# Optimization experiments

Measured on AMD Instinct MI355X. Metric: run time of the kernel, lower is better.

## Reference

```python
import jax, jax.numpy as jnp
import numpy as np

N = 16000      # points
K = 16         # neighbors per query (fixed-degree CSR)
M = N * K      # attention pairs
C = 384        # embed_dim
H = 6          # num_heads
HD = C // H    # head_dim = 64
L = 25         # quant_grid_length = window/quant = 6.0/0.24
T2 = 2 * L - 1 # rel-pos table length = 49
WIN = 6.0
QUANT = 0.24
SCALE = HD ** -0.5


def setup_inputs() -> dict:
    key = jax.random.key(0)
    ks = jax.random.split(key, 12)
    feats = jax.random.normal(ks[0], (N, C), jnp.float32)
    xyz = jax.random.uniform(ks[1], (N, 3), jnp.float32) * 240.0
    index_0 = jnp.repeat(jnp.arange(N, dtype=jnp.int32), K)            # sorted query ids per pair
    index_0_offsets = jnp.arange(0, M + 1, K, dtype=jnp.int32)         # CSR offsets
    index_1 = jax.random.randint(ks[2], (M,), 0, N, jnp.int32)         # key ids per pair
    sort_idx = jax.random.permutation(ks[3], N).astype(jnp.int32)
    lin = lambda k: jax.random.normal(k, (C, C), jnp.float32) * 0.02
    tab = lambda k: jax.random.normal(k, (T2, 3, H, HD), jnp.float32) * 0.02
    return {
        'feats': feats, 'xyz': xyz,
        'index_0': index_0, 'index_0_offsets': index_0_offsets,
        'index_1': index_1, 'sort_idx': sort_idx,
        'Wq': lin(ks[4]), 'bq': jnp.zeros((C,), jnp.float32),
        'Wk': lin(ks[5]), 'bk': jnp.zeros((C,), jnp.float32),
        'Wv': lin(ks[6]), 'bv': jnp.zeros((C,), jnp.float32),
        'Wp': lin(ks[7]), 'bp': jnp.zeros((C,), jnp.float32),
        'Tq': tab(ks[8]), 'Tk': tab(ks[9]), 'Tv': tab(ks[10]),
    }


def reference(feats, xyz, index_0, index_0_offsets, index_1, sort_idx,
              Wq, bq, Wk, bk, Wv, bv, Wp, bp, Tq, Tk, Tv):
    n = feats.shape[0]
    # QKV projections (key/value default to query feats in the module)
    q = (feats @ Wq.T + bq).reshape(n, H, HD) * SCALE
    k = (feats @ Wk.T + bk).reshape(n, H, HD)
    v = (feats @ Wv.T + bv).reshape(n, H, HD)
    # sort into contiguous-window order
    qs, ks_, vs = q[sort_idx], k[sort_idx], v[sort_idx]
    xyz_s = xyz[sort_idx]
    # quantized in-window coords (shift_win=False -> shift 0)
    xq = jnp.floor(((xyz_s - xyz_s.min(0)) % WIN) / QUANT)             # [N,3], values in [0, L-1]
    i0, i1 = index_0, index_1
    rel_idx = (xq[i0] - xq[i1]).astype(jnp.int32) + (L - 1)            # [M,3] in [0, 2L-2]
    # attention logits: q.k plus contextual relative-position terms
    attn = jnp.einsum('mhd,mhd->mh', qs[i0], ks_[i1])                  # [M,H]
    for t in range(3):
        dq = jnp.einsum('nhd,lhd->nlh', qs, Tq[:, t])                  # [N,T2,H]
        dk = jnp.einsum('nhd,lhd->nlh', ks_, Tk[:, t])
        attn = attn + dq[i0, rel_idx[:, t]] + dk[i1, rel_idx[:, t]]
    # scatter softmax over CSR segments (segments given by index_0)
    amax = jax.ops.segment_max(attn, i0, num_segments=n)
    e = jnp.exp(attn - amax[i0])
    denom = jax.ops.segment_sum(e, i0, num_segments=n)
    a = e / denom[i0]                                                  # [M,H]
    # weighted value aggregation
    x = jax.ops.segment_sum(a[:, :, None] * vs[i1], i0, num_segments=n)  # [N,H,HD]
    # relative-position value contribution, factored through table bins
    for t in range(3):
        seg2 = i0 * T2 + rel_idx[:, t]
        w = jax.ops.segment_sum(a, seg2, num_segments=n * T2).reshape(n, T2, H)
        x = x + jnp.einsum('nlh,lhd->nhd', w, Tv[:, t])
    # unsort back to input order and project
    out = jnp.zeros_like(x).at[sort_idx].set(x).reshape(n, C)
    return out @ Wp.T + bp
```

## Files before the change

### kernel.cpp

```cpp
#include <hip/hip_runtime.h>
#include <hip/hip_bf16.h>
#include <cstdint>
#include <cstddef>

#define NPTS 16000
#define KNB  16
#define CDIM 384
#define NH   6
#define HDIM 64
#define T2C  49
#define NL3T 147
#define THR  160
#define NXC  1152
#define KVROW 384

static constexpr float WIN    = 6.0f;
static constexpr float QUANT  = 0.24f;
static constexpr float QSCALE = 0.125f;
static constexpr float DQS    = 8.0f;
static constexpr float DQSINV = 0.125f;

typedef __attribute__((ext_vector_type(8))) short short8;
typedef __attribute__((ext_vector_type(4))) float floatx4;
typedef __attribute__((ext_vector_type(4))) unsigned short ushort4v;
typedef __attribute__((ext_vector_type(2))) float float2v;

__device__ inline unsigned short f2bf(float x) {
    unsigned int u = __float_as_uint(x);
    unsigned int r = (u + 0x7fffu + ((u >> 16) & 1u)) >> 16;
    return (unsigned short)r;
}
__device__ inline float bf2f(unsigned short b) {
    return __uint_as_float(((unsigned int)b) << 16);
}
__device__ inline float f8tof(unsigned char b) {
    return __builtin_amdgcn_cvt_f32_fp8((int)b, 0);
}
__device__ inline float2v bfpair(unsigned int w) {
    float2v r;
    r.x = __uint_as_float(w << 16);
    r.y = __uint_as_float(w & 0xffff0000u);
    return r;
}

__device__ inline void swz_nh(int& nb, int& h) {
    const int gx   = gridDim.x;
    const int nwg  = gx * NH;
    const int orig = blockIdx.y * gx + blockIdx.x;
    const int q    = nwg >> 3, r = nwg & 7;
    const int xcd  = orig & 7, idx = orig >> 3;
    const int wg   = (xcd < r ? xcd * (q + 1) : r * (q + 1) + (xcd - r) * q) + idx;
    h  = wg / gx;
    nb = wg % gx;
}

__global__ void min_kernel(const float* __restrict__ xyz,
                           unsigned int* __restrict__ minbits) {
    float m0 = INFINITY, m1 = INFINITY, m2 = INFINITY;
    for (int i = blockIdx.x * blockDim.x + threadIdx.x; i < NPTS;
         i += gridDim.x * blockDim.x) {
        m0 = fminf(m0, xyz[i * 3 + 0]);
        m1 = fminf(m1, xyz[i * 3 + 1]);
        m2 = fminf(m2, xyz[i * 3 + 2]);
    }
#pragma unroll
    for (int off = 1; off < 64; off <<= 1) {
        m0 = fminf(m0, __shfl_xor(m0, off, 64));
        m1 = fminf(m1, __shfl_xor(m1, off, 64));
        m2 = fminf(m2, __shfl_xor(m2, off, 64));
    }
    if ((threadIdx.x & 63) == 0) {
        atomicMin(&minbits[0], __float_as_uint(m0));
        atomicMin(&minbits[1], __float_as_uint(m1));
        atomicMin(&minbits[2], __float_as_uint(m2));
    }
}

__global__ void xq_kernel(const float* __restrict__ xyz,
                          const int* __restrict__ sort_idx,
                          const unsigned int* __restrict__ minbits,
                          int* __restrict__ xq) {
    int n = blockIdx.x * blockDim.x + threadIdx.x;
    if (n >= NPTS) return;
    int orig = sort_idx[n];
#pragma unroll
    for (int t = 0; t < 3; ++t) {
        float mn = __uint_as_float(minbits[t]);
        float v  = xyz[orig * 3 + t] - mn;
        float md = fmodf(v, WIN);
        float q  = floorf(md / QUANT);
        xq[n * 3 + t] = (int)q;
    }
}

__global__ void relpack_kernel(const int* __restrict__ idx1,
                               const int* __restrict__ xq,
                               unsigned int* __restrict__ pairs) {
    int m = blockIdx.x * blockDim.x + threadIdx.x;
    if (m >= NPTS * KNB) return;
    int n = m >> 4;
    int key = idx1[m];
    int r0 = xq[n * 3 + 0] - xq[key * 3 + 0] + 24; r0 = min(max(r0, 0), T2C - 1);
    int r1 = xq[n * 3 + 1] - xq[key * 3 + 1] + 24; r1 = min(max(r1, 0), T2C - 1);
    int r2 = xq[n * 3 + 2] - xq[key * 3 + 2] + 24; r2 = min(max(r2, 0), T2C - 1);
    pairs[m] = (unsigned)key | ((unsigned)r0 << 14) | ((unsigned)r1 << 20) |
               ((unsigned)r2 << 26);
}

#define G0 (NPTS * CDIM / 4)
#define G1 (3 * CDIM * CDIM)
#define G2 (CDIM * CDIM)
#define G3 (NH * THR * HDIM)
#define G6 (NH * THR * HDIM)
#define G7 (NH * THR * HDIM)
#define G4 (3 * CDIM)
#define G5 (CDIM)
__global__ void prep_kernel(const float* __restrict__ feats,
                            const int* __restrict__ sortix,
                            const float* __restrict__ Wq,
                            const float* __restrict__ Wk,
                            const float* __restrict__ Wv,
                            const float* __restrict__ Wp,
                            const float* __restrict__ bq,
                            const float* __restrict__ bk,
                            const float* __restrict__ bv,
                            const float* __restrict__ bp,
                            const float* __restrict__ Tv,
                            const float* __restrict__ Tq,
                            const float* __restrict__ Tk,
                            unsigned short* __restrict__ featsbf,
                            unsigned short* __restrict__ Wall,
                            unsigned short* __restrict__ Wpbf,
                            float* __restrict__ Tvh,
                            unsigned short* __restrict__ Tqh,
                            unsigned short* __restrict__ Tkh,
                            float* __restrict__ bfull,
                            float* __restrict__ bproj) {
    int i = blockIdx.x * blockDim.x + threadIdx.x;
    if (i < G0) {
        int n  = i / (CDIM / 4);
        int c4 = (i % (CDIM / 4)) * 4;
        const float4 v = *(const float4*)&feats[(size_t)sortix[n] * CDIM + c4];
        ushort4v o;
        o.x = f2bf(v.x); o.y = f2bf(v.y); o.z = f2bf(v.z); o.w = f2bf(v.w);
        *(ushort4v*)&featsbf[(size_t)n * CDIM + c4] = o;
        return;
    }
    i -= G0;
    if (i < G1) {
        int j = i / CDIM, k = i % CDIM;
        float v = (j < 384) ? Wq[j * CDIM + k]
                : (j < 768) ? Wk[(j - 384) * CDIM + k]
                            : Wv[(j - 768) * CDIM + k];
        Wall[i] = f2bf(v);
        return;
    }
    i -= G1;
    if (i < G2) { Wpbf[i] = f2bf(Wp[i]); return; }
    i -= G2;
    if (i < G3) {
        int jr = (i / HDIM) % THR, d = i % HDIM, h = i / (THR * HDIM);
        Tvh[i] = (jr < NL3T) ? Tv[(size_t)(jr * 6 + h) * HDIM + d] : 0.0f;
        return;
    }
    i -= G3;
    if (i < G6) {
        int jr = (i / HDIM) % THR, d = i % HDIM, h = i / (THR * HDIM);
        Tqh[i] = (jr < NL3T) ? f2bf(Tq[(size_t)(jr * 6 + h) * HDIM + d])
                             : (unsigned short)0;
        return;
    }
    i -= G6;
    if (i < G7) {
        int jr = (i / HDIM) % THR, d = i % HDIM, h = i / (THR * HDIM);
        Tkh[i] = (jr < NL3T) ? f2bf(Tk[(size_t)(jr * 6 + h) * HDIM + d])
                             : (unsigned short)0;
        return;
    }
    i -= G7;
    if (i < G4) {
        bfull[i] = (i < 384) ? bq[i] : (i < 768) ? bk[i - 384] : bv[i - 768];
        return;
    }
    i -= G4;
    if (i < G5) { bproj[i] = bp[i]; }
}

__global__ __launch_bounds__(256) void gemm_big(
    const unsigned short* __restrict__ Abf,
    const unsigned short* __restrict__ Wmat,
    const float* __restrict__ bias,
    int mode,
    unsigned char* __restrict__ qh8, unsigned char* __restrict__ kvh8,
    float* __restrict__ outf) {
    __shared__ unsigned short As[128 * 64];
    __shared__ unsigned short Bs[128 * 64];
    const int tid  = threadIdx.x;
    const int lane = tid & 63;
    const int w    = tid >> 6;
    const int wm   = w >> 1, wn = w & 1;

    const int nwg  = gridDim.x * gridDim.y;
    const int orig = blockIdx.y * gridDim.x + blockIdx.x;
    const int qq   = nwg >> 3, rr = nwg & 7;
    const int xcd  = orig & 7, idx = orig >> 3;
    const int wg   = (xcd < rr ? xcd * (qq + 1) : rr * (qq + 1) + (xcd - rr) * qq) + idx;
    const int jn0  = (wg % gridDim.x) * 128;
    const int m0   = (wg / gridDim.x) * 128;

    floatx4 acc[4][4];
#pragma unroll
    for (int i = 0; i < 4; ++i)
#pragma unroll
        for (int j = 0; j < 4; ++j) acc[i][j] = (floatx4)0.0f;

    for (int kt = 0; kt < 6; ++kt) {
        const int k0 = kt * 64;
#pragma unroll
        for (int q = 0; q < 4; ++q) {
            const int s    = w * 4 + q;
            const int row  = s * 8 + (lane >> 3);
            const int col  = (lane & 7) * 8;
            const unsigned short* ga = Abf  + (size_t)(m0  + row) * CDIM + k0 + col;
            const unsigned short* gb = Wmat + (size_t)(jn0 + row) * CDIM + k0 + col;
            __builtin_amdgcn_global_load_lds(
                (const __attribute__((address_space(1))) void*)ga,
                (__attribute__((address_space(3))) void*)&As[s * 512], 16, 0, 0);
            __builtin_amdgcn_global_load_lds(
                (const __attribute__((address_space(1))) void*)gb,
                (__attribute__((address_space(3))) void*)&Bs[s * 512], 16, 0, 0);
        }
        __syncthreads();
#pragma unroll
        for (int ks = 0; ks < 2; ++ks) {
            short8 a[4], b[4];
#pragma unroll
            for (int mi = 0; mi < 4; ++mi) {
                int row = wm * 64 + mi * 16 + (lane & 15);
                a[mi] = *(const short8*)&As[row * 64 + ks * 32 + (lane >> 4) * 8];
            }
#pragma unroll
            for (int ni = 0; ni < 4; ++ni) {
                int jr = wn * 64 + ni * 16 + (lane & 15);
                b[ni] = *(const short8*)&Bs[jr * 64 + ks * 32 + (lane >> 4) * 8];
            }
#pragma unroll
            for (int mi = 0; mi < 4; ++mi)
#pragma unroll
                for (int ni = 0; ni < 4; ++ni)
                    acc[mi][ni] = __builtin_amdgcn_mfma_f32_16x16x32_bf16(
                        b[ni], a[mi], acc[mi][ni], 0, 0, 0);
        }
        __syncthreads();
    }

#pragma unroll
    for (int mi = 0; mi < 4; ++mi) {
        const int n = m0 + wm * 64 + mi * 16 + (lane & 15);
#pragma unroll
        for (int ni = 0; ni < 4; ++ni) {
            const int jjb = jn0 + wn * 64 + ni * 16 + (lane >> 4) * 4;
            const float4 b4 = *(const float4*)&bias[jjb];
            const float v0 = acc[mi][ni][0] + b4.x;
            const float v1 = acc[mi][ni][1] + b4.y;
            const float v2 = acc[mi][ni][2] + b4.z;
            const float v3 = acc[mi][ni][3] + b4.w;
            if (mode == 0) {
                if (jjb < 384) {
                    const int h = jjb >> 6, d = jjb & 63;
                    ushort4v o;
                    o.x = f2bf(v0 * QSCALE); o.y = f2bf(v1 * QSCALE);
                    o.z = f2bf(v2 * QSCALE); o.w = f2bf(v3 * QSCALE);
                    *(ushort4v*)(qh8 + ((size_t)h * NPTS + n) * 128 + d * 2) = o;
                } else if (jjb < 768) {
                    const int jj = jjb - 384;
                    const int h = jj >> 6, d = jj & 63;
                    ushort4v o;
                    o.x = f2bf(v0); o.y = f2bf(v1);
                    o.z = f2bf(v2); o.w = f2bf(v3);
                    *(ushort4v*)(kvh8 + ((size_t)h * NPTS + n) * KVROW + d * 2) = o;
                } else {
                    const int jj = jjb - 768;
                    const int h = jj >> 6, d = jj & 63;
                    float4 o; o.x = v0; o.y = v1; o.z = v2; o.w = v3;
                    *(float4*)(kvh8 + ((size_t)h * NPTS + n) * KVROW + 128 + d * 4) = o;
                }
            } else {
                float4 o; o.x = v0; o.y = v1; o.z = v2; o.w = v3;
                *(float4*)&outf[(size_t)n * CDIM + jjb] = o;
            }
        }
    }
}

__global__ __launch_bounds__(256) void dqdk_kernel(
    const unsigned char* __restrict__ qh8,
    const unsigned char* __restrict__ kvh8,
    const unsigned short* __restrict__ Tqh,
    const unsigned short* __restrict__ Tkh,
    unsigned char* __restrict__ dqh,
    unsigned char* __restrict__ dkh) {
    __shared__ unsigned short As[128 * 64];
    __shared__ unsigned short Bs[THR * 64];
    const int tid  = threadIdx.x;
    const int lane = tid & 63;
    const int w    = tid >> 6;
    const int wm   = w >> 1, wn = w & 1;
    const int h    = blockIdx.y;
    const bool isk = blockIdx.z != 0;
    const unsigned char* srcb = isk ? kvh8 + (size_t)h * NPTS * KVROW
                                    : qh8  + (size_t)h * NPTS * 128;
    const int sstride = isk ? KVROW : 128;
    unsigned char* dst = (isk ? dkh : dqh) + (size_t)h * NPTS * THR;
    const unsigned short* T = (isk ? Tkh : Tqh) + (size_t)h * THR * HDIM;
    const int m0 = blockIdx.x * 128;

#pragma unroll
    for (int q = 0; q < 4; ++q) {
        const int s   = w * 4 + q;
        const int row = s * 8 + (lane >> 3);
        const unsigned char* ga = srcb + (size_t)(m0 + row) * sstride + (lane & 7) * 16;
        __builtin_amdgcn_global_load_lds(
            (const __attribute__((address_space(1))) void*)ga,
            (__attribute__((address_space(3))) void*)&As[s * 512], 16, 0, 0);
    }
#pragma unroll
    for (int q = 0; q < 5; ++q) {
        const int s   = w * 5 + q;
        const int row = s * 8 + (lane >> 3);
        const unsigned short* gb = T + (size_t)row * HDIM + (lane & 7) * 8;
        __builtin_amdgcn_global_load_lds(
            (const __attribute__((address_space(1))) void*)gb,
            (__attribute__((address_space(3))) void*)&Bs[s * 512], 16, 0, 0);
    }
    __syncthreads();

    floatx4 acc[4][5];
#pragma unroll
    for (int i = 0; i < 4; ++i)
#pragma unroll
        for (int j = 0; j < 5; ++j) acc[i][j] = (floatx4)0.0f;

#pragma unroll
    for (int ks = 0; ks < 2; ++ks) {
        short8 a[4], b[5];
#pragma unroll
        for (int mi = 0; mi < 4; ++mi) {
            int row = wm * 64 + mi * 16 + (lane & 15);
            a[mi] = *(const short8*)&As[row * 64 + ks * 32 + (lane >> 4) * 8];
        }
#pragma unroll
        for (int ni = 0; ni < 5; ++ni) {
            int jr = wn * 80 + ni * 16 + (lane & 15);
            b[ni] = *(const short8*)&Bs[jr * 64 + ks * 32 + (lane >> 4) * 8];
        }
#pragma unroll
        for (int mi = 0; mi < 4; ++mi)
#pragma unroll
            for (int ni = 0; ni < 5; ++ni)
                acc[mi][ni] = __builtin_amdgcn_mfma_f32_16x16x32_bf16(
                    b[ni], a[mi], acc[mi][ni], 0, 0, 0);
    }

#pragma unroll
    for (int mi = 0; mi < 4; ++mi) {
        const int n = m0 + wm * 64 + mi * 16 + (lane & 15);
#pragma unroll
        for (int ni = 0; ni < 5; ++ni) {
            const int jr0 = wn * 80 + ni * 16 + (lane >> 4) * 4;
            int u = __builtin_amdgcn_cvt_pk_fp8_f32(acc[mi][ni][0] * DQS,
                                                    acc[mi][ni][1] * DQS, 0, false);
            u = __builtin_amdgcn_cvt_pk_fp8_f32(acc[mi][ni][2] * DQS,
                                                acc[mi][ni][3] * DQS, u, true);
            *(unsigned int*)(dst + (size_t)n * THR + jr0) = (unsigned)u;
        }
    }
}

__global__ __launch_bounds__(256) void tqk_kernel(
    const unsigned int* __restrict__ pairs,
    const unsigned char* __restrict__ dqh,
    const unsigned char* __restrict__ dkh,
    unsigned short* __restrict__ tqk) {
    int nb, h;
    swz_nh(nb, h);
    const int n = nb * 4 + (threadIdx.x >> 6);
    const int lane = threadIdx.x & 63;
    const int p = lane >> 2, s = lane & 3;

    const unsigned int pv = pairs[n * KNB + p];
    float v = 0.0f;
    if (s < 3) {
        const int key = (int)(pv & 0x3FFFu);
        const int r = (int)((pv >> (14 + 6 * s)) & 63u);
        const int jr = r * 3 + s;
        v = f8tof(dqh[(size_t)h * NPTS * THR + (size_t)n * THR + jr]) +
            f8tof(dkh[(size_t)h * NPTS * THR + (size_t)key * THR + jr]);
    }
    v += __shfl_xor(v, 1, 64);
    v += __shfl_xor(v, 2, 64);
    if (s == 0)
        tqk[((size_t)h * NPTS + n) * KNB + p] = f2bf(v * DQSINV);
}

__global__ __launch_bounds__(256) void attn_kernel(
    const unsigned char* __restrict__ qh8,
    const unsigned char* __restrict__ kvh8,
    const unsigned int* __restrict__ pairs,
    const unsigned short* __restrict__ tqk,
    const float* __restrict__ Tvh,
    const int* __restrict__ sortix,
    unsigned short* __restrict__ xb) {
    int nb, h;
    swz_nh(nb, h);
    const int n = nb * 4 + (threadIdx.x >> 6);
    const int lane = threadIdx.x & 63;
    const int pp = lane >> 4, c = lane & 15;
    const int c8 = c * 8;

    const unsigned char* kvb = kvh8 + (size_t)h * NPTS * KVROW;
    const float* Tvb = Tvh + (size_t)h * THR * HDIM;
    const unsigned short* tqr = tqk + ((size_t)h * NPTS + n) * KNB;

    const uint2 qw = *(const uint2*)(qh8 + ((size_t)h * NPTS + n) * 128 + c8);
    const float2v q01 = bfpair(qw.x), q23 = bfpair(qw.y);

    unsigned int pv[4];
#pragma unroll
    for (int g = 0; g < 4; ++g) pv[g] = pairs[n * KNB + g * 4 + pp];

    int kbase[4], t0o[4], t1o[4], t2o[4];
#pragma unroll
    for (int g = 0; g < 4; ++g) {
        kbase[g] = (int)(pv[g] & 0x3FFFu) * KVROW;
        t0o[g]  = (int)((pv[g] >> 14) & 63u) * 192 + c * 4;
        t1o[g]  = (int)((pv[g] >> 20) & 63u) * 192 + 64 + c * 4;
        t2o[g]  = (int)(pv[g] >> 26) * 192 + 128 + c * 4;
    }

    float lg[4];
#pragma unroll
    for (int g = 0; g < 4; ++g) {
        const uint2 kw = *(const uint2*)(kvb + kbase[g] + c8);
        float2v d = q01 * bfpair(kw.x) + q23 * bfpair(kw.y);
        lg[g] = d.x + d.y;
    }
#pragma unroll
    for (int m = 1; m <= 8; m <<= 1)
#pragma unroll
        for (int g = 0; g < 4; ++g) lg[g] += __shfl_xor(lg[g], m, 64);
#pragma unroll
    for (int g = 0; g < 4; ++g) lg[g] += bf2f(tqr[g * 4 + pp]);

    float mx = fmaxf(fmaxf(lg[0], lg[1]), fmaxf(lg[2], lg[3]));
    mx = fmaxf(mx, __shfl_xor(mx, 16, 64));
    mx = fmaxf(mx, __shfl_xor(mx, 32, 64));
    float e[4], s = 0.f;
#pragma unroll
    for (int g = 0; g < 4; ++g) { e[g] = expf(lg[g] - mx); s += e[g]; }
    s += __shfl_xor(s, 16, 64);
    s += __shfl_xor(s, 32, 64);
    const float inv = 1.f / s;

    floatx4 xa = (floatx4)0.0f;
#pragma unroll
    for (int g = 0; g < 4; ++g) {
        const float wgt = e[g] * inv;
        const floatx4 vv = *(const floatx4*)(kvb + kbase[g] + 128 + c * 16);
        const floatx4 a0 = *(const floatx4*)&Tvb[t0o[g]];
        const floatx4 a1 = *(const floatx4*)&Tvb[t1o[g]];
        const floatx4 a2 = *(const floatx4*)&Tvb[t2o[g]];
        xa += wgt * (vv + a0 + a1 + a2);
    }
    float xa0 = xa[0], xa1 = xa[1], xa2 = xa[2], xa3 = xa[3];
#pragma unroll
    for (int m = 16; m <= 32; m <<= 1) {
        xa0 += __shfl_xor(xa0, m, 64);
        xa1 += __shfl_xor(xa1, m, 64);
        xa2 += __shfl_xor(xa2, m, 64);
        xa3 += __shfl_xor(xa3, m, 64);
    }
    if (pp == 0) {
        const int dst = sortix[n];
        ushort4v o;
        o.x = f2bf(xa0); o.y = f2bf(xa1); o.z = f2bf(xa2); o.w = f2bf(xa3);
        *(ushort4v*)&xb[(size_t)dst * CDIM + h * HDIM + c * 4] = o;
    }
}

extern "C" void kernel_launch(void* const* d_in, const int* in_sizes, int n_in,
                              void* d_out, int out_size, void* d_ws,
                              size_t ws_size, hipStream_t stream) {
    const float* feats  = (const float*)d_in[0];
    const float* xyz    = (const float*)d_in[1];
    const int*   index1 = (const int*)d_in[4];
    const int*   sortix = (const int*)d_in[5];
    const float* Wq = (const float*)d_in[6];
    const float* bq = (const float*)d_in[7];
    const float* Wk = (const float*)d_in[8];
    const float* bk = (const float*)d_in[9];
    const float* Wv = (const float*)d_in[10];
    const float* bv = (const float*)d_in[11];
    const float* Wp = (const float*)d_in[12];
    const float* bp = (const float*)d_in[13];
    const float* Tq = (const float*)d_in[14];
    const float* Tk = (const float*)d_in[15];
    const float* Tv = (const float*)d_in[16];
    float* out = (float*)d_out;

    char* ws = (char*)d_ws;
    size_t off = 0;
    auto alloc = [&](size_t bytes) -> void* {
        void* p = ws + off;
        off = (off + bytes + 255) & ~(size_t)255;
        return p;
    };
    unsigned short* featsbf = (unsigned short*)alloc((size_t)NPTS * CDIM * 2);
    unsigned short* Wall    = (unsigned short*)alloc((size_t)NXC * CDIM * 2);
    unsigned short* Wpbf    = (unsigned short*)alloc((size_t)CDIM * CDIM * 2);
    float*          Tvh     = (float*)alloc((size_t)NH * THR * HDIM * 4);
    unsigned short* Tqh     = (unsigned short*)alloc((size_t)NH * THR * HDIM * 2);
    unsigned short* Tkh     = (unsigned short*)alloc((size_t)NH * THR * HDIM * 2);
    float*          bfull   = (float*)alloc((size_t)NXC * sizeof(float));
    float*          bproj   = (float*)alloc((size_t)CDIM * sizeof(float));
    unsigned char*  qh8     = (unsigned char*)alloc((size_t)NH * NPTS * 128);
    unsigned char*  kvh8    = (unsigned char*)alloc((size_t)NH * NPTS * KVROW);
    unsigned char*  dqh     = (unsigned char*)alloc((size_t)NH * NPTS * THR);
    unsigned char*  dkh     = (unsigned char*)alloc((size_t)NH * NPTS * THR);
    unsigned short* tqk     = (unsigned short*)alloc((size_t)NH * NPTS * KNB * 2);
    unsigned int*   pairs   = (unsigned int*)alloc((size_t)NPTS * KNB * 4);
    int*            xq      = (int*)alloc((size_t)NPTS * 3 * sizeof(int));
    unsigned int*   minbits = (unsigned int*)alloc(16);
    unsigned short* xb      = featsbf;

    hipMemsetAsync(minbits, 0x7f, 16, stream);
    min_kernel<<<128, 256, 0, stream>>>(xyz, minbits);
    xq_kernel<<<(NPTS + 255) / 256, 256, 0, stream>>>(xyz, sortix, minbits, xq);
    relpack_kernel<<<(NPTS * KNB + 255) / 256, 256, 0, stream>>>(index1, xq, pairs);

    const int prep_total = G0 + G1 + G2 + G3 + G6 + G7 + G4 + G5;
    prep_kernel<<<(prep_total + 255) / 256, 256, 0, stream>>>(
        feats, sortix, Wq, Wk, Wv, Wp, bq, bk, bv, bp, Tv, Tq, Tk,
        featsbf, Wall, Wpbf, Tvh, Tqh, Tkh, bfull, bproj);

    dim3 g0(NXC / 128, NPTS / 128);
    gemm_big<<<g0, 256, 0, stream>>>(featsbf, Wall, bfull, 0, qh8, kvh8,
                                     (float*)nullptr);

    dim3 gd(NPTS / 128, NH, 2);
    dqdk_kernel<<<gd, 256, 0, stream>>>(qh8, kvh8, Tqh, Tkh, dqh, dkh);

    dim3 ga(NPTS / 4, NH);
    tqk_kernel<<<ga, 256, 0, stream>>>(pairs, dqh, dkh, tqk);

    attn_kernel<<<ga, 256, 0, stream>>>(qh8, kvh8, pairs, tqk, Tvh, sortix, xb);

    dim3 g1(CDIM / 128, NPTS / 128);
    gemm_big<<<g1, 256, 0, stream>>>(xb, Wpbf, bproj, 1, (unsigned char*)nullptr,
                                     (unsigned char*)nullptr, out);
}
```

Measured before the change: 211.0 us.

## Interleave bf16 K and V per row and store V as bf16 for attention gathers

Shrinks each per-head K/V row from 384 to 256 bytes by storing V in bf16 instead of fp32. K and V are interleaved in 4-element chunks so the attention kernel gets a lane's K and V slice from one 16-byte gather per neighbor instead of two separate loads. A separate contiguous bf16 K buffer is also written for the dqdk GEMM, which adds an extra store in the QKV GEMM epilogue. It also swaps in fast exp and a hardware reciprocal in the softmax, with some loss of V precision and accuracy.

```diff
diff --git a/kernel.cpp b/kernel.cpp
--- a/kernel.cpp
+++ b/kernel.cpp
@@ -12,7 +12,7 @@
 #define NL3T 147
 #define THR  160
 #define NXC  1152
-#define KVROW 384
+#define KVROW 256
 
 static constexpr float WIN    = 6.0f;
 static constexpr float QUANT  = 0.24f;
@@ -191,8 +191,8 @@
     const unsigned short* __restrict__ Wmat,
     const float* __restrict__ bias,
     int mode,
-    unsigned char* __restrict__ qh8, unsigned char* __restrict__ kvh8,
-    float* __restrict__ outf) {
+    unsigned char* __restrict__ qh8, unsigned char* __restrict__ kh8,
+    unsigned char* __restrict__ kvh8, float* __restrict__ outf) {
     __shared__ unsigned short As[128 * 64];
     __shared__ unsigned short Bs[128 * 64];
     const int tid  = threadIdx.x;
@@ -278,12 +278,15 @@
                     ushort4v o;
                     o.x = f2bf(v0); o.y = f2bf(v1);
                     o.z = f2bf(v2); o.w = f2bf(v3);
-                    *(ushort4v*)(kvh8 + ((size_t)h * NPTS + n) * KVROW + d * 2) = o;
+                    *(ushort4v*)(kh8 + ((size_t)h * NPTS + n) * 128 + d * 2) = o;
+                    *(ushort4v*)(kvh8 + ((size_t)h * NPTS + n) * KVROW + d * 4) = o;
                 } else {
                     const int jj = jjb - 768;
                     const int h = jj >> 6, d = jj & 63;
-                    float4 o; o.x = v0; o.y = v1; o.z = v2; o.w = v3;
-                    *(float4*)(kvh8 + ((size_t)h * NPTS + n) * KVROW + 128 + d * 4) = o;
+                    ushort4v o;
+                    o.x = f2bf(v0); o.y = f2bf(v1);
+                    o.z = f2bf(v2); o.w = f2bf(v3);
+                    *(ushort4v*)(kvh8 + ((size_t)h * NPTS + n) * KVROW + d * 4 + 8) = o;
                 }
             } else {
                 float4 o; o.x = v0; o.y = v1; o.z = v2; o.w = v3;
@@ -295,7 +298,7 @@
 
 __global__ __launch_bounds__(256) void dqdk_kernel(
     const unsigned char* __restrict__ qh8,
-    const unsigned char* __restrict__ kvh8,
+    const unsigned char* __restrict__ kh8,
     const unsigned short* __restrict__ Tqh,
     const unsigned short* __restrict__ Tkh,
     unsigned char* __restrict__ dqh,
@@ -308,9 +311,7 @@
     const int wm   = w >> 1, wn = w & 1;
     const int h    = blockIdx.y;
     const bool isk = blockIdx.z != 0;
-    const unsigned char* srcb = isk ? kvh8 + (size_t)h * NPTS * KVROW
-                                    : qh8  + (size_t)h * NPTS * 128;
-    const int sstride = isk ? KVROW : 128;
+    const unsigned char* srcb = (isk ? kh8 : qh8) + (size_t)h * NPTS * 128;
     unsigned char* dst = (isk ? dkh : dqh) + (size_t)h * NPTS * THR;
     const unsigned short* T = (isk ? Tkh : Tqh) + (size_t)h * THR * HDIM;
     const int m0 = blockIdx.x * 128;
@@ -319,7 +320,7 @@
     for (int q = 0; q < 4; ++q) {
         const int s   = w * 4 + q;
         const int row = s * 8 + (lane >> 3);
-        const unsigned char* ga = srcb + (size_t)(m0 + row) * sstride + (lane & 7) * 16;
+        const unsigned char* ga = srcb + (size_t)(m0 + row) * 128 + (lane & 7) * 16;
         __builtin_amdgcn_global_load_lds(
             (const __attribute__((address_space(1))) void*)ga,
             (__attribute__((address_space(3))) void*)&As[s * 512], 16, 0, 0);
@@ -416,34 +417,31 @@
     const int n = nb * 4 + (threadIdx.x >> 6);
     const int lane = threadIdx.x & 63;
     const int pp = lane >> 4, c = lane & 15;
-    const int c8 = c * 8;
 
     const unsigned char* kvb = kvh8 + (size_t)h * NPTS * KVROW;
     const float* Tvb = Tvh + (size_t)h * THR * HDIM;
     const unsigned short* tqr = tqk + ((size_t)h * NPTS + n) * KNB;
 
-    const uint2 qw = *(const uint2*)(qh8 + ((size_t)h * NPTS + n) * 128 + c8);
+    const uint2 qw = *(const uint2*)(qh8 + ((size_t)h * NPTS + n) * 128 + c * 8);
     const float2v q01 = bfpair(qw.x), q23 = bfpair(qw.y);
 
     unsigned int pv[4];
 #pragma unroll
     for (int g = 0; g < 4; ++g) pv[g] = pairs[n * KNB + g * 4 + pp];
 
-    int kbase[4], t0o[4], t1o[4], t2o[4];
+    int t0o[4], t1o[4], t2o[4];
+    uint2 vw[4];
+    float lg[4];
 #pragma unroll
     for (int g = 0; g < 4; ++g) {
-        kbase[g] = (int)(pv[g] & 0x3FFFu) * KVROW;
-        t0o[g]  = (int)((pv[g] >> 14) & 63u) * 192 + c * 4;
-        t1o[g]  = (int)((pv[g] >> 20) & 63u) * 192 + 64 + c * 4;
-        t2o[g]  = (int)(pv[g] >> 26) * 192 + 128 + c * 4;
-    }
-
-    float lg[4];
-#pragma unroll
-    for (int g = 0; g < 4; ++g) {
-        const uint2 kw = *(const uint2*)(kvb + kbase[g] + c8);
-        float2v d = q01 * bfpair(kw.x) + q23 * bfpair(kw.y);
+        t0o[g] = (int)((pv[g] >> 14) & 63u) * 192 + c * 4;
+        t1o[g] = (int)((pv[g] >> 20) & 63u) * 192 + 64 + c * 4;
+        t2o[g] = (int)(pv[g] >> 26) * 192 + 128 + c * 4;
+        const uint4 kv4 =
+            *(const uint4*)(kvb + (int)(pv[g] & 0x3FFFu) * KVROW + c * 16);
+        float2v d = q01 * bfpair(kv4.x) + q23 * bfpair(kv4.y);
         lg[g] = d.x + d.y;
+        vw[g].x = kv4.z; vw[g].y = kv4.w;
     }
 #pragma unroll
     for (int m = 1; m <= 8; m <<= 1)
@@ -457,16 +455,18 @@
     mx = fmaxf(mx, __shfl_xor(mx, 32, 64));
     float e[4], s = 0.f;
 #pragma unroll
-    for (int g = 0; g < 4; ++g) { e[g] = expf(lg[g] - mx); s += e[g]; }
+    for (int g = 0; g < 4; ++g) { e[g] = __expf(lg[g] - mx); s += e[g]; }
     s += __shfl_xor(s, 16, 64);
     s += __shfl_xor(s, 32, 64);
-    const float inv = 1.f / s;
+    const float inv = __builtin_amdgcn_rcpf(s);
 
     floatx4 xa = (floatx4)0.0f;
 #pragma unroll
     for (int g = 0; g < 4; ++g) {
         const float wgt = e[g] * inv;
-        const floatx4 vv = *(const floatx4*)(kvb + kbase[g] + 128 + c * 16);
+        const float2v v01 = bfpair(vw[g].x), v23 = bfpair(vw[g].y);
+        floatx4 vv;
+        vv[0] = v01.x; vv[1] = v01.y; vv[2] = v23.x; vv[3] = v23.y;
         const floatx4 a0 = *(const floatx4*)&Tvb[t0o[g]];
         const floatx4 a1 = *(const floatx4*)&Tvb[t1o[g]];
         const floatx4 a2 = *(const floatx4*)&Tvb[t2o[g]];
@@ -524,6 +524,7 @@
     float*          bfull   = (float*)alloc((size_t)NXC * sizeof(float));
     float*          bproj   = (float*)alloc((size_t)CDIM * sizeof(float));
     unsigned char*  qh8     = (unsigned char*)alloc((size_t)NH * NPTS * 128);
+    unsigned char*  kh8     = (unsigned char*)alloc((size_t)NH * NPTS * 128);
     unsigned char*  kvh8    = (unsigned char*)alloc((size_t)NH * NPTS * KVROW);
     unsigned char*  dqh     = (unsigned char*)alloc((size_t)NH * NPTS * THR);
     unsigned char*  dkh     = (unsigned char*)alloc((size_t)NH * NPTS * THR);
@@ -544,11 +545,11 @@
         featsbf, Wall, Wpbf, Tvh, Tqh, Tkh, bfull, bproj);
 
     dim3 g0(NXC / 128, NPTS / 128);
-    gemm_big<<<g0, 256, 0, stream>>>(featsbf, Wall, bfull, 0, qh8, kvh8,
+    gemm_big<<<g0, 256, 0, stream>>>(featsbf, Wall, bfull, 0, qh8, kh8, kvh8,
                                      (float*)nullptr);
 
     dim3 gd(NPTS / 128, NH, 2);
-    dqdk_kernel<<<gd, 256, 0, stream>>>(qh8, kvh8, Tqh, Tkh, dqh, dkh);
+    dqdk_kernel<<<gd, 256, 0, stream>>>(qh8, kh8, Tqh, Tkh, dqh, dkh);
 
     dim3 ga(NPTS / 4, NH);
     tqk_kernel<<<ga, 256, 0, stream>>>(pairs, dqh, dkh, tqk);
@@ -557,5 +558,6 @@
 
     dim3 g1(CDIM / 128, NPTS / 128);
     gemm_big<<<g1, 256, 0, stream>>>(xb, Wpbf, bproj, 1, (unsigned char*)nullptr,
-                                     (unsigned char*)nullptr, out);
-}
+                                     (unsigned char*)nullptr, (unsigned char*)nullptr,
+                                     out);
+}
```

New measurement: 203.6 us. 1.04x faster.
